# Kernel tuning notes

Hardware: AMD Instinct MI355X
Metric: run time of the kernel (lower is better)

Reference implementation:

```python
import jax, jax.numpy as jnp
import numpy as np

N_ANCH = 8400      # YOLOv8 anchors for 640x640
NUM_CLS = 600
H_IMG = 640
W_IMG = 640
PRE_NMS = 1024     # fixed pre-NMS pool (replaces dynamic NMS input size)
M_MAX = 31         # fixed max surviving detections (padded)
OUT = 224
SCORE_THRESH = 0.1
IOU_THRESH = 0.45
SCALES = jnp.array([0.7071, 1.0, 1.4142], jnp.float32)
MEAN = jnp.array([0.485, 0.456, 0.406], jnp.float32).reshape(1, 3, 1, 1)
STD = jnp.array([0.229, 0.224, 0.225], jnp.float32).reshape(1, 3, 1, 1)
ALLOWED = [41, 68, 70, 74, 87, 95, 113, 144, 150, 158, 164, 165, 193, 205, 212, 224,
           257, 298, 310, 335, 351, 354, 390, 393, 401, 403, 439, 442, 457, 466, 489,
           510, 512, 514, 524, 530, 531, 543, 546, 554, 565, 573, 580, 587, 588, 591]


def setup_inputs() -> dict:
    key = jax.random.key(0)
    k1, k2, k3, k4 = jax.random.split(key, 4)
    # box channels: cx,cy in pixel coords; w,h in [20, 200] px
    cxcy = jax.random.uniform(k1, (1, 2, N_ANCH), jnp.float32) * jnp.array([W_IMG, H_IMG], jnp.float32).reshape(1, 2, 1)
    wh = jax.random.uniform(k2, (1, 2, N_ANCH), jnp.float32) * 180.0 + 20.0
    logits = jax.random.uniform(k3, (1, NUM_CLS, N_ANCH), jnp.float32)
    raw_pred = jnp.concatenate([cxcy, wh, logits], axis=1)
    image = jax.random.uniform(k4, (1, 3, H_IMG, W_IMG), jnp.float32)
    allowed_cl = jnp.array(ALLOWED, jnp.int32)
    return {"raw_pred": raw_pred, "image": image, "allowed_cl": allowed_cl}


def _pairwise_iou(b):
    # b: [P,4] (x1,y1,x2,y2) -> [P,P] IoU (torchvision convention, no +1)
    area = (b[:, 2] - b[:, 0]) * (b[:, 3] - b[:, 1])
    lt = jnp.maximum(b[:, None, :2], b[None, :, :2])   # [P,P,2]
    rb = jnp.minimum(b[:, None, 2:], b[None, :, 2:])
    wh = jnp.clip(rb - lt, 0.0)
    inter = wh[..., 0] * wh[..., 1]
    union = area[:, None] + area[None, :] - inter
    return inter / jnp.maximum(union, 1e-12)


def _greedy_nms(iou, thr):
    # boxes assumed pre-sorted by descending score
    n = iou.shape[0]
    rng = jnp.arange(n)

    def step(supp, i):
        keep_i = jnp.logical_not(supp[i])
        supp = supp | (keep_i & (iou[i] > thr) & (rng > i))
        return supp, keep_i

    _, keep = jax.lax.scan(step, jnp.zeros(n, bool), rng)
    return keep


def _crop_bilinear(img, box):
    # img: [3,H,W]; box: (x1,y1,x2,y2). roi_align, aligned=True, sampling_ratio=1.
    C, H, W = img.shape
    x1, y1, x2, y2 = box[0], box[1], box[2], box[3]
    bw = (x2 - x1) / OUT
    bh = (y2 - y1) / OUT
    r = jnp.arange(OUT, dtype=jnp.float32) + 0.5
    xs = x1 - 0.5 + r * bw
    ys = y1 - 0.5 + r * bh
    mx = (xs > -1.0) & (xs < W)
    my = (ys > -1.0) & (ys < H)
    xsc = jnp.clip(xs, 0.0, W - 1.0)
    ysc = jnp.clip(ys, 0.0, H - 1.0)
    y0 = jnp.floor(ysc).astype(jnp.int32)
    x0 = jnp.floor(xsc).astype(jnp.int32)
    y1i = jnp.minimum(y0 + 1, H - 1)
    x1i = jnp.minimum(x0 + 1, W - 1)
    wy = ysc - y0.astype(jnp.float32)
    wx = xsc - x0.astype(jnp.float32)
    # separable bilinear: interp rows along y, then columns along x
    rows = img[:, y0, :] * (1.0 - wy)[None, :, None] + img[:, y1i, :] * wy[None, :, None]  # [3,OUT,W]
    out = rows[:, :, x0] * (1.0 - wx)[None, None, :] + rows[:, :, x1i] * wx[None, None, :]  # [3,OUT,OUT]
    return out * (my[None, :, None] & mx[None, None, :]).astype(img.dtype)


def reference(raw_pred, image, allowed_cl):
    x = raw_pred[0].T                            # [N, 4+C]
    cx, cy, w, h = x[:, 0], x[:, 1], x[:, 2], x[:, 3]
    boxes = jnp.stack([cx - w * 0.5, cy - h * 0.5, cx + w * 0.5, cy + h * 0.5], axis=1)
    logits = x[:, 4:]
    scores = logits.max(axis=1)
    classes = logits.argmax(axis=1).astype(jnp.int32)

    # fixed-size pre-NMS pool, sorted by descending score
    sc, idx = jax.lax.top_k(scores, PRE_NMS)
    b = boxes[idx]
    cl = classes[idx]

    keep = _greedy_nms(_pairwise_iou(b), IOU_THRESH)
    in_allowed = (cl[:, None] == allowed_cl[None, :].astype(cl.dtype)).any(axis=1)
    valid = keep & (sc > SCORE_THRESH) & in_allowed

    masked = jnp.where(valid, sc, -jnp.inf)
    topv, topi = jax.lax.top_k(masked, M_MAX)
    sel_valid = topv > -jnp.inf
    sel_boxes = jnp.where(sel_valid[:, None], b[topi], 0.0)
    sel_scores = jnp.where(sel_valid, sc[topi], 0.0)
    sel_cls = jnp.where(sel_valid, cl[topi], 0)

    full_box = jnp.array([[0.0, 0.0, W_IMG - 1.0, H_IMG - 1.0]], jnp.float32)
    final_boxes = jnp.concatenate([full_box, sel_boxes], axis=0)            # [M+1,4]
    final_scores = jnp.concatenate([jnp.ones((1,), jnp.float32), sel_scores])
    final_classes = jnp.concatenate([-jnp.ones((1,), cl.dtype), sel_cls])

    # multi-scale boxes, same center, clamped to image
    bx1, by1, bx2, by2 = (final_boxes[:, i] for i in range(4))
    ccx = (bx1 + bx2) * 0.5
    ccy = (by1 + by2) * 0.5
    ww = (bx2 - bx1)[:, None] * SCALES[None, :] * 0.5
    hh = (by2 - by1)[:, None] * SCALES[None, :] * 0.5
    scaled = jnp.stack([
        jnp.clip(ccx[:, None] - ww, 0.0, W_IMG - 1.0),
        jnp.clip(ccy[:, None] - hh, 0.0, H_IMG - 1.0),
        jnp.clip(ccx[:, None] + ww, 0.0, W_IMG - 1.0),
        jnp.clip(ccy[:, None] + hh, 0.0, H_IMG - 1.0),
    ], axis=-1)                                                             # [M+1,K,4]

    boxes_flat = scaled.reshape(-1, 4)                                      # [(M+1)*K,4]
    crops = jax.vmap(lambda bb: _crop_bilinear(image[0], bb))(boxes_flat)   # [(M+1)*K,3,224,224]
    crops_norm = (crops - MEAN) / STD
    return final_boxes, final_scores, final_classes, crops_norm
```

## Files before the change

### kernel.cpp

```cpp
#include <hip/hip_runtime.h>
#include <hip/hip_bf16.h>
#include <stdint.h>

#define N_ANCH   8400
#define NUM_CLS  600
#define H_IMG    640
#define W_IMG    640
#define PRE_NMS  1024
#define M_MAX    31
#define OUT_SZ   224
#define SCORE_THRESH 0.1f
#define IOU_THRESH   0.45f

__global__ __launch_bounds__(512) void k_prep(
    const float* __restrict__ raw,
    float* __restrict__ x1, float* __restrict__ y1,
    float* __restrict__ x2, float* __restrict__ y2,
    float* __restrict__ sc, int* __restrict__ cls) {
  __shared__ float s_m[8][64];
  __shared__ int   s_mi[8][64];
  const int lane = threadIdx.x & 63;
  const int part = threadIdx.x >> 6;
  const int a = blockIdx.x * 64 + lane;

  float m = -INFINITY; int mi = 0;
  if (a < N_ANCH) {
    const float* lp = raw + (size_t)(4 + part * 75) * N_ANCH + a;
    #pragma unroll 5
    for (int cc = 0; cc < 75; ++cc) {
      float v = lp[(size_t)cc * N_ANCH];
      if (v > m) { m = v; mi = part * 75 + cc; }
    }
  }
  s_m[part][lane] = m; s_mi[part][lane] = mi;
  __syncthreads();
  if (part == 0 && a < N_ANCH) {
    #pragma unroll
    for (int p = 1; p < 8; ++p) {
      float vm = s_m[p][lane];
      if (vm > m) { m = vm; mi = s_mi[p][lane]; }
    }
    sc[a] = m; cls[a] = mi;
    float cx = raw[a];
    float cy = raw[(size_t)1 * N_ANCH + a];
    float w  = raw[(size_t)2 * N_ANCH + a];
    float h  = raw[(size_t)3 * N_ANCH + a];
    x1[a] = cx - w * 0.5f; y1[a] = cy - h * 0.5f;
    x2[a] = cx + w * 0.5f; y2[a] = cy + h * 0.5f;
  }
}

__device__ __forceinline__ unsigned long long shflxor64(unsigned long long v, int j) {
  int lo = __shfl_xor((int)(unsigned int)v, j, 64);
  int hi = __shfl_xor((int)(unsigned int)(v >> 32), j, 64);
  return ((unsigned long long)(unsigned int)hi << 32) | (unsigned int)lo;
}

__global__ __launch_bounds__(1024) void k_select(
    const float* __restrict__ sc, const int* __restrict__ cls,
    const float* __restrict__ x1, const float* __restrict__ y1,
    const float* __restrict__ x2, const float* __restrict__ y2,
    float* __restrict__ t_sc, float* __restrict__ tb, int* __restrict__ t_cl) {
  __shared__ unsigned int hist[8][2048];
  __shared__ unsigned long long C[N_ANCH];
  __shared__ unsigned long long s_sel[PRE_NMS];
  __shared__ unsigned int wt[16];
  __shared__ int s_bstar, s_above, s_cnt;
  __shared__ unsigned long long s_thr;

  const int tid = threadIdx.x;
  const int lane = tid & 63, wid = tid >> 6;
  unsigned int* hf = &hist[0][0];

  unsigned long long ka[9];
  bool kv[9];
  #pragma unroll
  for (int e = 0; e < 9; ++e) {
    int a = tid + e * 1024;
    kv[e] = (a < N_ANCH);
    float s = kv[e] ? sc[a] : 0.0f;
    ka[e] = (((unsigned long long)__float_as_uint(s)) << 32) |
            (unsigned long long)(0xFFFFFFFFu - (unsigned)a);
  }

  int need = PRE_NMS;
  unsigned long long thr = 0ULL;
  int m = 0;

  #pragma unroll
  for (int i = tid; i < 8 * 2048; i += 1024) hf[i] = 0;
  if (tid == 0) s_cnt = 0;
  __syncthreads();
  #pragma unroll
  for (int e = 0; e < 9; ++e)
    if (kv[e]) atomicAdd(&hist[wid & 7][(unsigned)((ka[e] >> 51) & 2047ULL)], 1u);
  __syncthreads();
  {
    unsigned int h0 = 0, h1 = 0;
    #pragma unroll
    for (int cp = 0; cp < 8; ++cp) { h0 += hist[cp][2 * tid]; h1 += hist[cp][2 * tid + 1]; }
    unsigned int suf = h0 + h1;
    #pragma unroll
    for (int o = 1; o < 64; o <<= 1) {
      unsigned int t = __shfl_down(suf, o, 64);
      if (lane + o < 64) suf += t;
    }
    if (lane == 0) wt[wid] = suf;
    __syncthreads();
    unsigned int add = 0;
    #pragma unroll
    for (int q = 0; q < 16; ++q) if (q > wid) add += wt[q];
    const unsigned int S0 = suf + add, S1 = S0 - h0, S2 = S1 - h1;
    if ((int)S0 >= need && (int)S1 < need) { s_bstar = 2 * tid;     s_above = (int)S1; }
    if ((int)S1 >= need && (int)S2 < need) { s_bstar = 2 * tid + 1; s_above = (int)S2; }
  }
  __syncthreads();
  {
    const int bstar = s_bstar;
    need -= s_above;
    thr |= (unsigned long long)bstar << 51;
    #pragma unroll
    for (int e = 0; e < 9; ++e)
      if (kv[e] && (int)((ka[e] >> 51) & 2047ULL) == bstar)
        C[atomicAdd(&s_cnt, 1)] = ka[e];
  }
  __syncthreads();
  m = s_cnt;

  const int shifts[5] = {40, 29, 18, 7, 0};
  for (int si = 0; si < 5 && m > 64; ++si) {
    const int shift = shifts[si];
    unsigned long long cu[9];
    #pragma unroll
    for (int e = 0; e < 9; ++e) {
      int i = tid + e * 1024;
      cu[e] = (i < m) ? C[i] : 0ULL;
    }
    #pragma unroll
    for (int i = tid; i < 8 * 2048; i += 1024) hf[i] = 0;
    if (tid == 0) s_cnt = 0;
    __syncthreads();
    #pragma unroll
    for (int e = 0; e < 9; ++e)
      if (tid + e * 1024 < m)
        atomicAdd(&hist[wid & 7][(unsigned)((cu[e] >> shift) & 2047ULL)], 1u);
    __syncthreads();
    {
      unsigned int h0 = 0, h1 = 0;
      #pragma unroll
      for (int cp = 0; cp < 8; ++cp) { h0 += hist[cp][2 * tid]; h1 += hist[cp][2 * tid + 1]; }
      unsigned int suf = h0 + h1;
      #pragma unroll
      for (int o = 1; o < 64; o <<= 1) {
        unsigned int t = __shfl_down(suf, o, 64);
        if (lane + o < 64) suf += t;
      }
      if (lane == 0) wt[wid] = suf;
      __syncthreads();
      unsigned int add = 0;
      #pragma unroll
      for (int q = 0; q < 16; ++q) if (q > wid) add += wt[q];
      const unsigned int S0 = suf + add, S1 = S0 - h0, S2 = S1 - h1;
      if ((int)S0 >= need && (int)S1 < need) { s_bstar = 2 * tid;     s_above = (int)S1; }
      if ((int)S1 >= need && (int)S2 < need) { s_bstar = 2 * tid + 1; s_above = (int)S2; }
    }
    __syncthreads();
    {
      const int bstar = s_bstar;
      need -= s_above;
      thr |= (unsigned long long)bstar << shift;
      #pragma unroll
      for (int e = 0; e < 9; ++e)
        if (tid + e * 1024 < m && (int)((cu[e] >> shift) & 2047ULL) == bstar)
          C[atomicAdd(&s_cnt, 1)] = cu[e];
    }
    __syncthreads();
    m = s_cnt;
  }

  if (wid == 0) {
    unsigned long long v = (lane < m) ? C[lane] : 0ULL;
    for (int k2 = 2; k2 <= 64; k2 <<= 1) {
      for (int j = k2 >> 1; j > 0; j >>= 1) {
        unsigned long long pv = shflxor64(v, j);
        bool keepmax = (((lane & k2) == 0) == ((lane & j) == 0));
        if (keepmax == (pv > v)) v = pv;
      }
    }
    if (lane == need - 1) s_thr = v;
  }
  if (tid == 0) s_cnt = 0;
  __syncthreads();

  const unsigned long long thrv = s_thr;
  #pragma unroll
  for (int e = 0; e < 9; ++e)
    if (kv[e] && ka[e] >= thrv) {
      int p = atomicAdd(&s_cnt, 1);
      if (p < PRE_NMS) s_sel[p] = ka[e];
    }
  __syncthreads();

  unsigned long long v = s_sel[tid];
  for (int k2 = 2; k2 <= PRE_NMS; k2 <<= 1) {
    for (int j = k2 >> 1; j > 0; j >>= 1) {
      unsigned long long pv;
      if (j >= 64) {
        __syncthreads();
        C[tid] = v;
        __syncthreads();
        pv = C[tid ^ j];
      } else {
        pv = shflxor64(v, j);
      }
      bool keepmax = (((tid & k2) == 0) == ((tid & j) == 0));
      if (keepmax == (pv > v)) v = pv;
    }
  }

  const int idx = (int)(0xFFFFFFFFu - (unsigned)(v & 0xFFFFFFFFULL));
  t_sc[tid] = __uint_as_float((unsigned)(v >> 32));
  tb[tid]               = x1[idx];
  tb[PRE_NMS + tid]     = y1[idx];
  tb[2 * PRE_NMS + tid] = x2[idx];
  tb[3 * PRE_NMS + tid] = y2[idx];
  t_cl[tid] = cls[idx];
}

__global__ __launch_bounds__(256) void k_iou_mask(
    const float* __restrict__ tb, unsigned long long* __restrict__ mask) {
  __shared__ float bx1[PRE_NMS], by1[PRE_NMS], bx2[PRE_NMS], by2[PRE_NMS], bar[PRE_NMS];
  const int tid = threadIdx.x;
  for (int a = tid; a < PRE_NMS; a += 256) {
    float X1 = tb[a], Y1 = tb[PRE_NMS + a], X2 = tb[2 * PRE_NMS + a], Y2 = tb[3 * PRE_NMS + a];
    bx1[a] = X1; by1[a] = Y1; bx2[a] = X2; by2[a] = Y2;
    bar[a] = (X2 - X1) * (Y2 - Y1);
  }
  __syncthreads();
  const int g = blockIdx.x * 256 + tid;
  const int i = g >> 4;
  const int w = g & 15;
  const float ix1 = bx1[i], iy1 = by1[i], ix2 = bx2[i], iy2 = by2[i], ia = bar[i];
  unsigned long long m = 0ULL;
  const int j0 = w * 64;
  #pragma unroll 8
  for (int l = 0; l < 64; ++l) {
    const int jj = (l + 4 * w) & 63;
    const int j = j0 + jj;
    float ltx = fmaxf(ix1, bx1[j]);
    float lty = fmaxf(iy1, by1[j]);
    float rbx = fminf(ix2, bx2[j]);
    float rby = fminf(iy2, by2[j]);
    float ww = fmaxf(rbx - ltx, 0.0f);
    float hh = fmaxf(rby - lty, 0.0f);
    float inter = ww * hh;
    float uni = ia + bar[j] - inter;
    float iou = inter / fmaxf(uni, 1e-12f);
    if (iou > IOU_THRESH && j > i) m |= (1ULL << jj);
  }
  mask[(size_t)i * 16 + w] = m;
}

__device__ __forceinline__ unsigned long long rdlane64(unsigned long long v, int lane) {
  unsigned int lo = (unsigned int)v;
  unsigned int hi = (unsigned int)(v >> 32);
  unsigned int a = (unsigned int)__builtin_amdgcn_readlane((int)lo, lane);
  unsigned int b = (unsigned int)__builtin_amdgcn_readlane((int)hi, lane);
  return ((unsigned long long)b << 32) | (unsigned long long)a;
}

__global__ __launch_bounds__(1024) void k_nms_final(
    const unsigned long long* __restrict__ mask,
    const float* __restrict__ t_sc, const float* __restrict__ tb,
    const int* __restrict__ t_cl, const int* __restrict__ allowed, int n_allowed,
    float* __restrict__ out, float* __restrict__ cropbox) {
  __shared__ unsigned long long L[PRE_NMS * 17];
  __shared__ unsigned long long s_keep[16];
  __shared__ unsigned long long s_wor[16];
  __shared__ unsigned long long s_albm[16];
  __shared__ int s_selr[M_MAX];
  __shared__ int s_nsel;
  const int tid = threadIdx.x;
  const int lane = tid & 63, wid = tid >> 6;

  const ulonglong2* m2 = (const ulonglong2*)mask;
  #pragma unroll
  for (int k = 0; k < 8; ++k) {
    int t2 = tid + k * 1024;
    ulonglong2 val = m2[t2];
    int row = t2 >> 3;
    int w0 = (t2 & 7) * 2;
    L[row * 17 + w0]     = val.x;
    L[row * 17 + w0 + 1] = val.y;
  }
  if (tid < 16) { s_keep[tid] = 0ULL; s_albm[tid] = 0ULL; }
  __syncthreads();
  if (tid < n_allowed) {
    int c = allowed[tid];
    atomicOr(&s_albm[c >> 6], 1ULL << (c & 63));
  }
  __syncthreads();

  for (int c = 0; c < 16; ++c) {
    unsigned long long v = 0ULL;
    if (tid < c * 64 && ((s_keep[tid >> 6] >> (unsigned)(tid & 63)) & 1ULL))
      v = L[tid * 17 + c];
    #pragma unroll
    for (int o = 1; o < 64; o <<= 1) v |= shflxor64(v, o);
    if (lane == 0) s_wor[wid] = v;
    __syncthreads();
    if (wid == 0) {
      unsigned long long pre = 0ULL;
      #pragma unroll
      for (int q = 0; q < 16; ++q) pre |= s_wor[q];
      unsigned long long d = L[(c * 64 + lane) * 17 + c];
      unsigned long long sup = pre, K = 0ULL;
      #pragma unroll
      for (int i = 0; i < 64; ++i) {
        unsigned long long di = rdlane64(d, i);
        unsigned long long nk = ((sup >> i) & 1ULL) ^ 1ULL;
        unsigned long long km = 0ULL - nk;
        K |= km & (1ULL << i);
        sup |= di & km;
      }
      if (lane == 0) s_keep[c] = K;
    }
    __syncthreads();
  }

  if (wid == 0) {
    bool validf[16];
    int cnt = 0;
    #pragma unroll
    for (int k = 0; k < 16; ++k) {
      const int r = lane * 16 + k;
      bool kp = ((s_keep[r >> 6] >> (unsigned)(r & 63)) & 1ULL) != 0ULL;
      float s = t_sc[r];
      int c = t_cl[r];
      bool ina = ((s_albm[c >> 6] >> (unsigned)(c & 63)) & 1ULL) != 0ULL;
      bool v = kp && (s > SCORE_THRESH) && ina;
      validf[k] = v;
      cnt += v ? 1 : 0;
    }
    int scan = cnt;
    #pragma unroll
    for (int o = 1; o < 64; o <<= 1) {
      int v = __shfl_up(scan, o, 64);
      if (lane >= o) scan += v;
    }
    const int excl = scan - cnt;
    int rk = excl;
    #pragma unroll
    for (int k = 0; k < 16; ++k) {
      if (validf[k]) {
        if (rk < M_MAX) s_selr[rk] = lane * 16 + k;
        rk++;
      }
    }
    if (lane == 63) s_nsel = (scan < M_MAX) ? scan : M_MAX;
  }
  __syncthreads();

  if (wid == 0 && lane < 32) {
    const int nsel = s_nsel;
    float b0, b1, b2, b3, fsc, fcl;
    if (lane == 0) {
      b0 = 0.0f; b1 = 0.0f; b2 = (float)(W_IMG - 1); b3 = (float)(H_IMG - 1);
      fsc = 1.0f; fcl = -1.0f;
    } else if (lane <= nsel) {
      int r = s_selr[lane - 1];
      b0 = tb[r]; b1 = tb[PRE_NMS + r]; b2 = tb[2 * PRE_NMS + r]; b3 = tb[3 * PRE_NMS + r];
      fsc = t_sc[r]; fcl = (float)t_cl[r];
    } else {
      b0 = b1 = b2 = b3 = 0.0f; fsc = 0.0f; fcl = 0.0f;
    }
    out[lane * 4 + 0] = b0; out[lane * 4 + 1] = b1;
    out[lane * 4 + 2] = b2; out[lane * 4 + 3] = b3;
    out[128 + lane] = fsc;
    out[160 + lane] = fcl;

    const float ccx = (b0 + b2) * 0.5f;
    const float ccy = (b1 + b3) * 0.5f;
    const float bwd = b2 - b0;
    const float bhd = b3 - b1;
    const float scl3[3] = {0.7071f, 1.0f, 1.4142f};
    #pragma unroll
    for (int s3 = 0; s3 < 3; ++s3) {
      float ww = bwd * scl3[s3] * 0.5f;
      float hh = bhd * scl3[s3] * 0.5f;
      float cx1 = fminf(fmaxf(ccx - ww, 0.0f), (float)(W_IMG - 1));
      float cy1 = fminf(fmaxf(ccy - hh, 0.0f), (float)(H_IMG - 1));
      float cx2 = fminf(fmaxf(ccx + ww, 0.0f), (float)(W_IMG - 1));
      float cy2 = fminf(fmaxf(ccy + hh, 0.0f), (float)(H_IMG - 1));
      const int bi = (lane * 3 + s3) * 4;
      cropbox[bi + 0] = cx1; cropbox[bi + 1] = cy1;
      cropbox[bi + 2] = cx2; cropbox[bi + 3] = cy2;
    }
  }
}

__global__ __launch_bounds__(256) void k_crop(
    const float* __restrict__ img, const float* __restrict__ cropbox,
    float* __restrict__ out) {
  const int gid = blockIdx.x * 256 + threadIdx.x;
  const int px = gid % OUT_SZ;
  const int t1 = gid / OUT_SZ;
  const int py = t1 % OUT_SZ;
  const int t2 = t1 / OUT_SZ;
  const int c = t2 % 3;
  const int b = t2 / 3;
  if (b >= 96) return;

  const float bx1 = cropbox[b * 4 + 0];
  const float by1 = cropbox[b * 4 + 1];
  const float bx2 = cropbox[b * 4 + 2];
  const float by2 = cropbox[b * 4 + 3];
  const float bw = (bx2 - bx1) / (float)OUT_SZ;
  const float bh = (by2 - by1) / (float)OUT_SZ;
  const float xs = bx1 - 0.5f + ((float)px + 0.5f) * bw;
  const float ys = by1 - 0.5f + ((float)py + 0.5f) * bh;
  const bool mx = (xs > -1.0f) && (xs < (float)W_IMG);
  const bool my = (ys > -1.0f) && (ys < (float)H_IMG);
  const float xsc = fminf(fmaxf(xs, 0.0f), (float)(W_IMG - 1));
  const float ysc = fminf(fmaxf(ys, 0.0f), (float)(H_IMG - 1));
  const int x0 = (int)floorf(xsc);
  const int y0 = (int)floorf(ysc);
  const int x1i = min(x0 + 1, W_IMG - 1);
  const int y1i = min(y0 + 1, H_IMG - 1);
  const float wx = xsc - (float)x0;
  const float wy = ysc - (float)y0;

  const float* ic = img + (size_t)c * (H_IMG * W_IMG);
  const float p00 = ic[y0 * W_IMG + x0];
  const float p01 = ic[y0 * W_IMG + x1i];
  const float p10 = ic[y1i * W_IMG + x0];
  const float p11 = ic[y1i * W_IMG + x1i];
  const float r0 = p00 * (1.0f - wy) + p10 * wy;
  const float r1 = p01 * (1.0f - wy) + p11 * wy;
  float v = r0 * (1.0f - wx) + r1 * wx;
  v = (mx && my) ? v : 0.0f;

  const float mean = (c == 0) ? 0.485f : ((c == 1) ? 0.456f : 0.406f);
  const float stdv = (c == 0) ? 0.229f : ((c == 1) ? 0.224f : 0.225f);
  out[gid] = (v - mean) / stdv;
}

extern "C" void kernel_launch(void* const* d_in, const int* in_sizes, int n_in,
                              void* d_out, int out_size, void* d_ws, size_t ws_size,
                              hipStream_t stream) {
  const float* raw = (const float*)d_in[0];
  const float* img = (const float*)d_in[1];
  const int* allowed = (const int*)d_in[2];
  float* out = (float*)d_out;

  unsigned long long* mask = (unsigned long long*)d_ws;
  float* fbase = (float*)((char*)d_ws + (size_t)PRE_NMS * 16 * 8);
  float* x1 = fbase + 0 * N_ANCH;
  float* y1 = fbase + 1 * N_ANCH;
  float* x2 = fbase + 2 * N_ANCH;
  float* y2 = fbase + 3 * N_ANCH;
  float* sc = fbase + 4 * N_ANCH;
  int*   cls = (int*)(fbase + 5 * N_ANCH);
  float* t_sc = fbase + 6 * N_ANCH;
  float* tb   = t_sc + PRE_NMS;
  int*   t_cl = (int*)(tb + 4 * PRE_NMS);
  float* cropbox = (float*)(t_cl + PRE_NMS);

  k_prep<<<(N_ANCH + 63) / 64, 512, 0, stream>>>(raw, x1, y1, x2, y2, sc, cls);
  k_select<<<1, 1024, 0, stream>>>(sc, cls, x1, y1, x2, y2, t_sc, tb, t_cl);
  k_iou_mask<<<64, 256, 0, stream>>>(tb, mask);
  k_nms_final<<<1, 1024, 0, stream>>>(mask, t_sc, tb, t_cl, allowed,
                                      in_sizes[2], out, cropbox);
  const int total = 96 * 3 * OUT_SZ * OUT_SZ;
  k_crop<<<(total + 255) / 256, 256, 0, stream>>>(img, cropbox, out + 192);
}
```

Before: 154.3 us.

## Distribute NMS suppression words per wave and vectorize crop output stores

The block-wide NMS loop no longer funnels every chunk through wave 0 with a shared OR-reduction. Each wave now keeps its own 64-bit suppression word and updates it after each resolved chunk, and wave c resolves chunk c. This cuts one barrier per iteration and the cross-wave reduction. The crop kernel now has each thread compute four horizontally adjacent output pixels, sharing the row setup across them, and writes them with a single float4 store, which reduces the thread count and gives wider global writes.

Measured after the change: 130.2 us. -15.6%, faster.

```diff
diff --git a/kernel.cpp b/kernel.cpp
--- a/kernel.cpp
+++ b/kernel.cpp
@@ -275,8 +275,7 @@
     const int* __restrict__ t_cl, const int* __restrict__ allowed, int n_allowed,
     float* __restrict__ out, float* __restrict__ cropbox) {
   __shared__ unsigned long long L[PRE_NMS * 17];
-  __shared__ unsigned long long s_keep[16];
-  __shared__ unsigned long long s_wor[16];
+  __shared__ unsigned long long s_K[16];
   __shared__ unsigned long long s_albm[16];
   __shared__ int s_selr[M_MAX];
   __shared__ int s_nsel;
@@ -293,40 +292,42 @@
     L[row * 17 + w0]     = val.x;
     L[row * 17 + w0 + 1] = val.y;
   }
-  if (tid < 16) { s_keep[tid] = 0ULL; s_albm[tid] = 0ULL; }
+  if (tid < 16) s_albm[tid] = 0ULL;
   __syncthreads();
   if (tid < n_allowed) {
     int c = allowed[tid];
     atomicOr(&s_albm[c >> 6], 1ULL << (c & 63));
   }
-  __syncthreads();
+
+  unsigned long long suppw = 0ULL;
 
   for (int c = 0; c < 16; ++c) {
-    unsigned long long v = 0ULL;
-    if (tid < c * 64 && ((s_keep[tid >> 6] >> (unsigned)(tid & 63)) & 1ULL))
-      v = L[tid * 17 + c];
-    #pragma unroll
-    for (int o = 1; o < 64; o <<= 1) v |= shflxor64(v, o);
-    if (lane == 0) s_wor[wid] = v;
-    __syncthreads();
-    if (wid == 0) {
-      unsigned long long pre = 0ULL;
-      #pragma unroll
-      for (int q = 0; q < 16; ++q) pre |= s_wor[q];
+    if (wid == c) {
       unsigned long long d = L[(c * 64 + lane) * 17 + c];
-      unsigned long long sup = pre, K = 0ULL;
+      unsigned int slo = (unsigned int)__builtin_amdgcn_readfirstlane((int)(unsigned int)suppw);
+      unsigned int shi = (unsigned int)__builtin_amdgcn_readfirstlane((int)(unsigned int)(suppw >> 32));
+      unsigned long long sup = ((unsigned long long)shi << 32) | slo;
+      unsigned long long K = 0ULL;
       #pragma unroll
       for (int i = 0; i < 64; ++i) {
         unsigned long long di = rdlane64(d, i);
-        unsigned long long nk = ((sup >> i) & 1ULL) ^ 1ULL;
-        unsigned long long km = 0ULL - nk;
-        K |= km & (1ULL << i);
-        sup |= di & km;
+        const bool kept = ((sup >> i) & 1ULL) == 0ULL;
+        K   |= kept ? (1ULL << i) : 0ULL;
+        sup |= kept ? di : 0ULL;
       }
-      if (lane == 0) s_keep[c] = K;
-    }
-    __syncthreads();
-  }
+      if (lane == 0) s_K[c] = K;
+    }
+    __syncthreads();
+    {
+      unsigned long long Kc = s_K[c];
+      unsigned long long v =
+          ((Kc >> (unsigned)lane) & 1ULL) ? L[(c * 64 + lane) * 17 + wid] : 0ULL;
+      #pragma unroll
+      for (int o = 1; o < 64; o <<= 1) v |= shflxor64(v, o);
+      suppw |= v;
+    }
+  }
+  __syncthreads();
 
   if (wid == 0) {
     bool validf[16];
@@ -334,7 +335,7 @@
     #pragma unroll
     for (int k = 0; k < 16; ++k) {
       const int r = lane * 16 + k;
-      bool kp = ((s_keep[r >> 6] >> (unsigned)(r & 63)) & 1ULL) != 0ULL;
+      bool kp = ((s_K[r >> 6] >> (unsigned)(r & 63)) & 1ULL) != 0ULL;
       float s = t_sc[r];
       int c = t_cl[r];
       bool ina = ((s_albm[c >> 6] >> (unsigned)(c & 63)) & 1ULL) != 0ULL;
@@ -403,8 +404,8 @@
     const float* __restrict__ img, const float* __restrict__ cropbox,
     float* __restrict__ out) {
   const int gid = blockIdx.x * 256 + threadIdx.x;
-  const int px = gid % OUT_SZ;
-  const int t1 = gid / OUT_SZ;
+  const int x4 = gid % (OUT_SZ / 4);
+  const int t1 = gid / (OUT_SZ / 4);
   const int py = t1 % OUT_SZ;
   const int t2 = t1 / OUT_SZ;
   const int c = t2 % 3;
@@ -417,32 +418,41 @@
   const float by2 = cropbox[b * 4 + 3];
   const float bw = (bx2 - bx1) / (float)OUT_SZ;
   const float bh = (by2 - by1) / (float)OUT_SZ;
-  const float xs = bx1 - 0.5f + ((float)px + 0.5f) * bw;
+
   const float ys = by1 - 0.5f + ((float)py + 0.5f) * bh;
-  const bool mx = (xs > -1.0f) && (xs < (float)W_IMG);
   const bool my = (ys > -1.0f) && (ys < (float)H_IMG);
-  const float xsc = fminf(fmaxf(xs, 0.0f), (float)(W_IMG - 1));
   const float ysc = fminf(fmaxf(ys, 0.0f), (float)(H_IMG - 1));
-  const int x0 = (int)floorf(xsc);
   const int y0 = (int)floorf(ysc);
-  const int x1i = min(x0 + 1, W_IMG - 1);
   const int y1i = min(y0 + 1, H_IMG - 1);
-  const float wx = xsc - (float)x0;
   const float wy = ysc - (float)y0;
 
-  const float* ic = img + (size_t)c * (H_IMG * W_IMG);
-  const float p00 = ic[y0 * W_IMG + x0];
-  const float p01 = ic[y0 * W_IMG + x1i];
-  const float p10 = ic[y1i * W_IMG + x0];
-  const float p11 = ic[y1i * W_IMG + x1i];
-  const float r0 = p00 * (1.0f - wy) + p10 * wy;
-  const float r1 = p01 * (1.0f - wy) + p11 * wy;
-  float v = r0 * (1.0f - wx) + r1 * wx;
-  v = (mx && my) ? v : 0.0f;
+  const float* r0p = img + (size_t)c * (H_IMG * W_IMG) + (size_t)y0 * W_IMG;
+  const float* r1p = img + (size_t)c * (H_IMG * W_IMG) + (size_t)y1i * W_IMG;
 
   const float mean = (c == 0) ? 0.485f : ((c == 1) ? 0.456f : 0.406f);
   const float stdv = (c == 0) ? 0.229f : ((c == 1) ? 0.224f : 0.225f);
-  out[gid] = (v - mean) / stdv;
+
+  auto pix = [&](int px) -> float {
+    const float xs = bx1 - 0.5f + ((float)px + 0.5f) * bw;
+    const bool mx = (xs > -1.0f) && (xs < (float)W_IMG);
+    const float xsc = fminf(fmaxf(xs, 0.0f), (float)(W_IMG - 1));
+    const int x0 = (int)floorf(xsc);
+    const int x1i = min(x0 + 1, W_IMG - 1);
+    const float wx = xsc - (float)x0;
+    const float r0 = r0p[x0] * (1.0f - wy) + r1p[x0] * wy;
+    const float r1 = r0p[x1i] * (1.0f - wy) + r1p[x1i] * wy;
+    float v = r0 * (1.0f - wx) + r1 * wx;
+    v = (mx && my) ? v : 0.0f;
+    return (v - mean) / stdv;
+  };
+
+  const int pxb = x4 * 4;
+  float4 res;
+  res.x = pix(pxb + 0);
+  res.y = pix(pxb + 1);
+  res.z = pix(pxb + 2);
+  res.w = pix(pxb + 3);
+  reinterpret_cast<float4*>(out)[gid] = res;
 }
 
 extern "C" void kernel_launch(void* const* d_in, const int* in_sizes, int n_in,
@@ -471,6 +481,6 @@
   k_iou_mask<<<64, 256, 0, stream>>>(tb, mask);
   k_nms_final<<<1, 1024, 0, stream>>>(mask, t_sc, tb, t_cl, allowed,
                                       in_sizes[2], out, cropbox);
-  const int total = 96 * 3 * OUT_SZ * OUT_SZ;
-  k_crop<<<(total + 255) / 256, 256, 0, stream>>>(img, cropbox, out + 192);
-}
+  const int total4 = 96 * 3 * OUT_SZ * OUT_SZ / 4;
+  k_crop<<<(total4 + 255) / 256, 256, 0, stream>>>(img, cropbox, out + 192);
+}
```
